# Kernel tuning notes

Measured on AMD Instinct MI355X. Metric: run time of the kernel, lower is better.

Reference implementation:

```python
import jax, jax.numpy as jnp
import numpy as np

B, IN_UNITS, IN_CH, NUM_UNITS, UNIT_SIZE = 32, 16, 2048, 16, 64
NUM_ITERS = 2


def setup_inputs() -> dict:
    key = jax.random.key(0)
    k1, k2 = jax.random.split(key)
    x = jax.random.normal(k1, (B, IN_UNITS, IN_CH), dtype=jnp.float32)
    W = jax.random.normal(k2, (1, IN_CH, NUM_UNITS, UNIT_SIZE, IN_UNITS), dtype=jnp.float32)
    return {"x": x, "W": W}


def squash(s):
    # torch code sums squared magnitude over dim=2 (the num_units axis) with keepdim
    mag_sq = jnp.sum(s * s, axis=2, keepdims=True)
    mag = jnp.sqrt(mag_sq)
    return mag_sq / (1.0 + mag_sq) * (s / mag)


def reference(x, W):
    # x: (B, in_units, in_channels) -> (B, in_channels, in_units)
    xt = jnp.swapaxes(x, 1, 2)
    # u_hat[b,i,j,k] = sum_u W[0,i,j,k,u] * xt[b,i,u]  -> (B, IC, NU, US)
    u_hat = jnp.einsum('ijku,biu->bijk', W[0], xt)
    b_ij = jnp.zeros((1, IN_CH, NUM_UNITS, 1), dtype=x.dtype)
    v_j = None
    for _ in range(NUM_ITERS):
        # softmax over a singleton trailing dim -> all ones (faithful to source)
        c_ij = jax.nn.softmax(b_ij, axis=-1)  # (1, IC, NU, 1), broadcasts over batch
        s_j = jnp.sum(c_ij[None, ..., 0][0][None].squeeze(0) * 0 + c_ij * u_hat, axis=1, keepdims=True) if False else jnp.sum(c_ij * u_hat, axis=1, keepdims=True)  # (B,1,NU,US)
        v_j = squash(s_j)  # (B,1,NU,US)
        # agreement: <u_hat, v_j> over unit_size, broadcast v_j over in_channels
        u_vj1 = jnp.einsum('bijk,bljk->bij', u_hat, v_j)  # (B, IC, NU)
        u_vj1 = jnp.mean(u_vj1, axis=0, keepdims=True)[..., None]  # (1, IC, NU, 1)
        b_ij = b_ij + u_vj1
    return v_j[:, 0, :, :]  # (B, num_units, unit_size)
```

## Files before the change

kernel.cpp:

```cpp
#include <hip/hip_runtime.h>
#include <hip/hip_bf16.h>


#define B_SZ   32
#define IC     2048
#define NJ     16
#define NK     64
#define SOUT   (B_SZ*NJ*NK)
#define KSTEPS 1024
#define KSPLIT 32
#define SPW    (KSTEPS/KSPLIT)

typedef float v4f __attribute__((ext_vector_type(4)));
typedef short v8s __attribute__((ext_vector_type(8)));

static __device__ inline ushort f2bf(float f) {
    uint32_t u = __float_as_uint(f);
    u += 0x7FFFu + ((u >> 16) & 1u);
    return (ushort)(u >> 16);
}

__global__ __launch_bounds__(256)
void caps_xprep(const float* __restrict__ x, ushort* __restrict__ xb) {
    int gid  = blockIdx.x * 256 + threadIdx.x;
    int lane = gid & 63;
    int mt   = (gid >> 6) & 1;
    int step = gid >> 7;
    int q    = lane >> 4;
    int b    = mt * 16 + (lane & 15);
    int i    = 2 * step + (q >> 1);
    int u0   = (q & 1) * 8;

    const float* xp = x + (size_t)b * (16 * IC) + (size_t)u0 * IC + i;
    ushort tmp[8];
    #pragma unroll
    for (int jj = 0; jj < 8; ++jj)
        tmp[jj] = f2bf(xp[(size_t)jj * IC]);
    *(v8s*)(xb + (size_t)gid * 8) = *(const v8s*)tmp;
}

__global__ __launch_bounds__(256)
void caps_mfma(const ushort* __restrict__ xb, const float* __restrict__ W,
               float* __restrict__ part) {
    const int tid   = threadIdx.x;
    const int wv    = tid >> 6;
    const int lane  = tid & 63;
    const int j     = blockIdx.x;
    const int split = blockIdx.y;
    const int n     = lane & 15;
    const int q     = lane >> 4;
    const int step0 = split * SPW;

    v4f acc0 = {0.f, 0.f, 0.f, 0.f};
    v4f acc1 = {0.f, 0.f, 0.f, 0.f};

    const float*  wp = W + (size_t)(2 * step0 + (q >> 1)) * 16384
                         + (size_t)j * 1024 + (size_t)(wv * 16 + n) * 16 + (q & 1) * 8;
    const ushort* xp = xb + (size_t)step0 * 1024 + (size_t)lane * 8;

    #pragma unroll 4
    for (int s = 0; s < SPW; ++s) {
        float4 w0 = *(const float4*)(wp);
        float4 w1 = *(const float4*)(wp + 4);
        v8s a0 = *(const v8s*)(xp);
        v8s a1 = *(const v8s*)(xp + 512);
        v8s bb;
        bb[0] = (short)f2bf(w0.x); bb[1] = (short)f2bf(w0.y);
        bb[2] = (short)f2bf(w0.z); bb[3] = (short)f2bf(w0.w);
        bb[4] = (short)f2bf(w1.x); bb[5] = (short)f2bf(w1.y);
        bb[6] = (short)f2bf(w1.z); bb[7] = (short)f2bf(w1.w);
        acc0 = __builtin_amdgcn_mfma_f32_16x16x32_bf16(a0, bb, acc0, 0, 0, 0);
        acc1 = __builtin_amdgcn_mfma_f32_16x16x32_bf16(a1, bb, acc1, 0, 0, 0);
        wp += 2 * 16384;
        xp += 1024;
    }

    float* pp = part + (size_t)split * SOUT + (size_t)j * NK + wv * 16 + n;
    #pragma unroll
    for (int r = 0; r < 4; ++r) {
        int m = q * 4 + r;
        pp[(size_t)m * 1024]        = acc0[r];
        pp[(size_t)(m + 16) * 1024] = acc1[r];
    }
}

__global__ __launch_bounds__(256)
void caps_finish(const float* __restrict__ part, float* __restrict__ out) {
    __shared__ float ls[256];
    const int blk = blockIdx.x;
    const int b   = blk >> 2;
    const int k0  = (blk & 3) * 16;
    const int t   = threadIdx.x;
    const int jj  = t >> 4;
    const int kc  = t & 15;
    const size_t idx = (size_t)b * 1024 + (size_t)jj * NK + k0 + kc;

    float s = 0.0f;
    #pragma unroll 8
    for (int sp = 0; sp < KSPLIT; ++sp)
        s += part[(size_t)sp * SOUT + idx];
    ls[t] = s;
    __syncthreads();

    float msq = 0.0f;
    #pragma unroll
    for (int j2 = 0; j2 < NJ; ++j2) {
        float v = ls[j2 * 16 + kc];
        msq += v * v;
    }
    float mag = sqrtf(msq);
    out[idx] = s * (mag / (1.0f + msq));
}

extern "C" void kernel_launch(void* const* d_in, const int* in_sizes, int n_in,
                              void* d_out, int out_size, void* d_ws, size_t ws_size,
                              hipStream_t stream) {
    const float* x = (const float*)d_in[0];
    const float* W = (const float*)d_in[1];
    float* out  = (float*)d_out;

    float*  part = (float*)d_ws;
    ushort* xb   = (ushort*)(part + (size_t)KSPLIT * SOUT);

    caps_xprep <<<512,               256, 0, stream>>>(x, xb);
    caps_mfma  <<<dim3(16, KSPLIT),  256, 0, stream>>>(xb, W, part);
    caps_finish<<<128,               256, 0, stream>>>(part, out);
}
```

Measured before the change: 202.7 us.

## Fuse prep, MFMA and finish stages into one cooperative kernel with grid syncs

Replaces the three separate launches (x conversion to bf16, split-K MFMA reduction, squash finish) with a single cooperative kernel of 512 blocks. Grid-wide syncs with thread fences separate the phases. The finish phase is re-partitioned so that every block takes part, with four threads per output sharing the split-sum reduction through shared memory. The aim is to remove launch gaps and spread the final reduction across more blocks. The cost is grid-sync overhead and a requirement that all blocks be co-resident.

```diff
diff --git a/kernel.cpp b/kernel.cpp
--- a/kernel.cpp
+++ b/kernel.cpp
@@ -1,5 +1,6 @@
 #include <hip/hip_runtime.h>
 #include <hip/hip_bf16.h>
+#include <hip/hip_cooperative_groups.h>
 
 
 #define B_SZ   32
@@ -21,95 +22,114 @@
 }
 
 __global__ __launch_bounds__(256)
-void caps_xprep(const float* __restrict__ x, ushort* __restrict__ xb) {
-    int gid  = blockIdx.x * 256 + threadIdx.x;
-    int lane = gid & 63;
-    int mt   = (gid >> 6) & 1;
-    int step = gid >> 7;
-    int q    = lane >> 4;
-    int b    = mt * 16 + (lane & 15);
-    int i    = 2 * step + (q >> 1);
-    int u0   = (q & 1) * 8;
+void caps_fused(const float* __restrict__ x, const float* __restrict__ W,
+                float* __restrict__ out, float* __restrict__ part,
+                ushort* __restrict__ xb) {
+    cooperative_groups::grid_group grid = cooperative_groups::this_grid();
+    const int tid = threadIdx.x;
+    const int bid = blockIdx.x;
 
-    const float* xp = x + (size_t)b * (16 * IC) + (size_t)u0 * IC + i;
-    ushort tmp[8];
-    #pragma unroll
-    for (int jj = 0; jj < 8; ++jj)
-        tmp[jj] = f2bf(xp[(size_t)jj * IC]);
-    *(v8s*)(xb + (size_t)gid * 8) = *(const v8s*)tmp;
-}
+    {
+        int gid  = bid * 256 + tid;
+        int lane = gid & 63;
+        int mt   = (gid >> 6) & 1;
+        int step = gid >> 7;
+        int q    = lane >> 4;
+        int b    = mt * 16 + (lane & 15);
+        int i    = 2 * step + (q >> 1);
+        int u0   = (q & 1) * 8;
 
-__global__ __launch_bounds__(256)
-void caps_mfma(const ushort* __restrict__ xb, const float* __restrict__ W,
-               float* __restrict__ part) {
-    const int tid   = threadIdx.x;
-    const int wv    = tid >> 6;
-    const int lane  = tid & 63;
-    const int j     = blockIdx.x;
-    const int split = blockIdx.y;
-    const int n     = lane & 15;
-    const int q     = lane >> 4;
-    const int step0 = split * SPW;
-
-    v4f acc0 = {0.f, 0.f, 0.f, 0.f};
-    v4f acc1 = {0.f, 0.f, 0.f, 0.f};
-
-    const float*  wp = W + (size_t)(2 * step0 + (q >> 1)) * 16384
-                         + (size_t)j * 1024 + (size_t)(wv * 16 + n) * 16 + (q & 1) * 8;
-    const ushort* xp = xb + (size_t)step0 * 1024 + (size_t)lane * 8;
-
-    #pragma unroll 4
-    for (int s = 0; s < SPW; ++s) {
-        float4 w0 = *(const float4*)(wp);
-        float4 w1 = *(const float4*)(wp + 4);
-        v8s a0 = *(const v8s*)(xp);
-        v8s a1 = *(const v8s*)(xp + 512);
-        v8s bb;
-        bb[0] = (short)f2bf(w0.x); bb[1] = (short)f2bf(w0.y);
-        bb[2] = (short)f2bf(w0.z); bb[3] = (short)f2bf(w0.w);
-        bb[4] = (short)f2bf(w1.x); bb[5] = (short)f2bf(w1.y);
-        bb[6] = (short)f2bf(w1.z); bb[7] = (short)f2bf(w1.w);
-        acc0 = __builtin_amdgcn_mfma_f32_16x16x32_bf16(a0, bb, acc0, 0, 0, 0);
-        acc1 = __builtin_amdgcn_mfma_f32_16x16x32_bf16(a1, bb, acc1, 0, 0, 0);
-        wp += 2 * 16384;
-        xp += 1024;
+        const float* xp = x + (size_t)b * (16 * IC) + (size_t)u0 * IC + i;
+        ushort tmp[8];
+        #pragma unroll
+        for (int jj = 0; jj < 8; ++jj)
+            tmp[jj] = f2bf(xp[(size_t)jj * IC]);
+        *(v8s*)(xb + (size_t)gid * 8) = *(const v8s*)tmp;
     }
 
-    float* pp = part + (size_t)split * SOUT + (size_t)j * NK + wv * 16 + n;
-    #pragma unroll
-    for (int r = 0; r < 4; ++r) {
-        int m = q * 4 + r;
-        pp[(size_t)m * 1024]        = acc0[r];
-        pp[(size_t)(m + 16) * 1024] = acc1[r];
+    __threadfence();
+    grid.sync();
+
+    {
+        const int wv    = tid >> 6;
+        const int lane  = tid & 63;
+        const int j     = bid & (NJ - 1);
+        const int split = bid >> 4;
+        const int n     = lane & 15;
+        const int q     = lane >> 4;
+        const int step0 = split * SPW;
+
+        v4f acc0 = {0.f, 0.f, 0.f, 0.f};
+        v4f acc1 = {0.f, 0.f, 0.f, 0.f};
+
+        const float*  wp = W + (size_t)(2 * step0 + (q >> 1)) * 16384
+                             + (size_t)j * 1024 + (size_t)(wv * 16 + n) * 16 + (q & 1) * 8;
+        const ushort* xp = xb + (size_t)step0 * 1024 + (size_t)lane * 8;
+
+        #pragma unroll 4
+        for (int s = 0; s < SPW; ++s) {
+            v4f w0 = *(const v4f*)(wp);
+            v4f w1 = *(const v4f*)(wp + 4);
+            v8s a0 = *(const v8s*)(xp);
+            v8s a1 = *(const v8s*)(xp + 512);
+            v8s bb;
+            bb[0] = (short)f2bf(w0.x); bb[1] = (short)f2bf(w0.y);
+            bb[2] = (short)f2bf(w0.z); bb[3] = (short)f2bf(w0.w);
+            bb[4] = (short)f2bf(w1.x); bb[5] = (short)f2bf(w1.y);
+            bb[6] = (short)f2bf(w1.z); bb[7] = (short)f2bf(w1.w);
+            acc0 = __builtin_amdgcn_mfma_f32_16x16x32_bf16(a0, bb, acc0, 0, 0, 0);
+            acc1 = __builtin_amdgcn_mfma_f32_16x16x32_bf16(a1, bb, acc1, 0, 0, 0);
+            wp += 2 * 16384;
+            xp += 1024;
+        }
+
+        float* pp = part + (size_t)split * SOUT + (size_t)j * NK + wv * 16 + n;
+        #pragma unroll
+        for (int r = 0; r < 4; ++r) {
+            int m = q * 4 + r;
+            pp[(size_t)m * 1024]        = acc0[r];
+            pp[(size_t)(m + 16) * 1024] = acc1[r];
+        }
     }
-}
 
-__global__ __launch_bounds__(256)
-void caps_finish(const float* __restrict__ part, float* __restrict__ out) {
-    __shared__ float ls[256];
-    const int blk = blockIdx.x;
-    const int b   = blk >> 2;
-    const int k0  = (blk & 3) * 16;
-    const int t   = threadIdx.x;
-    const int jj  = t >> 4;
-    const int kc  = t & 15;
-    const size_t idx = (size_t)b * 1024 + (size_t)jj * NK + k0 + kc;
+    __threadfence();
+    grid.sync();
 
-    float s = 0.0f;
-    #pragma unroll 8
-    for (int sp = 0; sp < KSPLIT; ++sp)
-        s += part[(size_t)sp * SOUT + idx];
-    ls[t] = s;
-    __syncthreads();
+    {
+        __shared__ float ls[256];
+        __shared__ float l2[64];
+        const int b  = bid >> 4;
+        const int k0 = (bid & 15) * 4;
+        const int jj = tid >> 4;
+        const int kc = (tid >> 2) & 3;
+        const int sg = tid & 3;
+        const size_t idx = (size_t)b * 1024 + (size_t)jj * NK + k0 + kc;
 
-    float msq = 0.0f;
-    #pragma unroll
-    for (int j2 = 0; j2 < NJ; ++j2) {
-        float v = ls[j2 * 16 + kc];
-        msq += v * v;
+        float s = 0.0f;
+        #pragma unroll
+        for (int ss = 0; ss < KSPLIT / 4; ++ss)
+            s += part[(size_t)(sg + 4 * ss) * SOUT + idx];
+        ls[tid] = s;
+        __syncthreads();
+
+        if (sg == 0) {
+            float sa = ls[tid] + ls[tid + 1] + ls[tid + 2] + ls[tid + 3];
+            l2[jj * 4 + kc] = sa;
+        }
+        __syncthreads();
+
+        if (sg == 0) {
+            float sa  = l2[jj * 4 + kc];
+            float msq = 0.0f;
+            #pragma unroll
+            for (int j2 = 0; j2 < NJ; ++j2) {
+                float v = l2[j2 * 4 + kc];
+                msq += v * v;
+            }
+            float mag = sqrtf(msq);
+            out[idx] = sa * (mag / (1.0f + msq));
+        }
     }
-    float mag = sqrtf(msq);
-    out[idx] = s * (mag / (1.0f + msq));
 }
 
 extern "C" void kernel_launch(void* const* d_in, const int* in_sizes, int n_in,
@@ -122,7 +142,7 @@
     float*  part = (float*)d_ws;
     ushort* xb   = (ushort*)(part + (size_t)KSPLIT * SOUT);
 
-    caps_xprep <<<512,               256, 0, stream>>>(x, xb);
-    caps_mfma  <<<dim3(16, KSPLIT),  256, 0, stream>>>(xb, W, part);
-    caps_finish<<<128,               256, 0, stream>>>(part, out);
+    void* args[] = {(void*)&x, (void*)&W, (void*)&out, (void*)&part, (void*)&xb};
+    hipLaunchCooperativeKernel((void*)caps_fused, dim3(NJ * KSPLIT), dim3(256),
+                               args, 0, stream);
 }
```

Measured after the change: 441.6 us. 2.18x slower.
